# Kernel optimization log

Measured on AMD Instinct MI355X. Metric: run time of the kernel, lower is better.

The kernel has to match this reference:

```python
import jax, jax.numpy as jnp
import numpy as np

D_MODEL = 1024
NUM_HEADS = 16
D_K = D_MODEL // NUM_HEADS
NEG_INF = -1.0e9


def setup_inputs() -> dict:
    key = jax.random.key(0)
    ks = jax.random.split(key, 12)
    B, S = 2, 2048
    s = 1.0 / np.sqrt(D_MODEL)
    return {
        "q": jax.random.normal(ks[0], (B, S, D_MODEL), jnp.float32),
        "k": jax.random.normal(ks[1], (B, S, D_MODEL), jnp.float32),
        "v": jax.random.normal(ks[2], (B, S, D_MODEL), jnp.float32),
        "encoder_mask": jnp.ones((B, 1, 1, S), jnp.int32),
        "W_q": jax.random.normal(ks[3], (D_MODEL, D_MODEL), jnp.float32) * s,
        "b_q": jnp.zeros((D_MODEL,), jnp.float32),
        "W_k": jax.random.normal(ks[4], (D_MODEL, D_MODEL), jnp.float32) * s,
        "b_k": jnp.zeros((D_MODEL,), jnp.float32),
        "W_v": jax.random.normal(ks[5], (D_MODEL, D_MODEL), jnp.float32) * s,
        "b_v": jnp.zeros((D_MODEL,), jnp.float32),
        "W_o": jax.random.normal(ks[6], (D_MODEL, D_MODEL), jnp.float32) * s,
        "b_o": jnp.zeros((D_MODEL,), jnp.float32),
    }


def reference(q, k, v, encoder_mask, W_q, b_q, W_k, b_k, W_v, b_v, W_o, b_o):
    B, S, _ = q.shape
    # projections (torch Linear: x @ W^T + b)
    def proj(x, W, b):
        y = x @ W.T + b
        return y.reshape(B, -1, NUM_HEADS, D_K).transpose(0, 2, 1, 3)  # [B,H,S,dk]

    Q = proj(q, W_q, b_q)
    K = proj(k, W_k, b_k)
    V = proj(v, W_v, b_v)

    scores = jnp.einsum("bhqd,bhkd->bhqk", Q, K) / jnp.sqrt(jnp.float32(D_K))
    scores = jnp.where(encoder_mask == 0, NEG_INF, scores)
    # NOTE: source module computes softmax(scores) but then (bug) multiplies
    # the raw masked scores by V; softmax result is dead code, so we skip it.
    attn_out = jnp.einsum("bhqk,bhkd->bhqd", scores, V)
    attn_out = attn_out.transpose(0, 2, 1, 3).reshape(B, S, D_MODEL)
    return attn_out @ W_o.T + b_o
```

## Files before the change

kernel.cpp:

```cpp
#include <hip/hip_runtime.h>
#include <stdint.h>

#define DM 1024
#define NH 16
#define DK 64

typedef __attribute__((ext_vector_type(8))) __bf16 bf16x8;
typedef __attribute__((ext_vector_type(4))) float f32x4;

__device__ __forceinline__ float bf2f(unsigned short u) {
    union { uint32_t i; float f; } x; x.i = ((uint32_t)u) << 16; return x.f;
}
__device__ __forceinline__ unsigned short f2bf(float f) {
    union { float f; uint32_t i; } x; x.f = f;
    uint32_t r = x.i + 0x7fffu + ((x.i >> 16) & 1u);
    return (unsigned short)(r >> 16);
}

__device__ __forceinline__ void gl2lds16(const void* g, void* l) {
    __builtin_amdgcn_global_load_lds(
        (const __attribute__((address_space(1))) void*)g,
        (__attribute__((address_space(3))) void*)l, 16, 0, 0);
}

__device__ __forceinline__ f32x4 mfma_bf16(bf16x8 a, bf16x8 b, f32x4 c) {
    return __builtin_amdgcn_mfma_f32_16x16x32_bf16(a, b, c, 0, 0, 0);
}

template<int N> __device__ __forceinline__ void waitvm() {
    if constexpr (N == 4)      asm volatile("s_waitcnt vmcnt(4)" ::: "memory");
    else if constexpr (N == 2) asm volatile("s_waitcnt vmcnt(2)" ::: "memory");
    else if constexpr (N == 0) asm volatile("s_waitcnt vmcnt(0)" ::: "memory");
}

struct CvtArgs {
    const float* src[15];
    unsigned short* dst[15];
};

__global__ __launch_bounds__(256) void cvt15(CvtArgs a) {
    const int t = blockIdx.x * 256 + threadIdx.x;
    const int seg = t >> 18;
    const int off = t & 0x3ffff;
    const float4 v = reinterpret_cast<const float4*>(a.src[seg])[off];
    ushort4 o;
    o.x = f2bf(v.x); o.y = f2bf(v.y); o.z = f2bf(v.z); o.w = f2bf(v.w);
    reinterpret_cast<ushort4*>(a.dst[seg])[off] = o;
}

template<typename OutT>
struct GKArgs {
    const unsigned short* A[3];
    const unsigned short* Wlo[3];
    const unsigned short* Whi[3];
    const float* blo[3];
    const float* bhi[3];
    OutT* C[3];
};

template<typename OutT>
__global__ __launch_bounds__(512, 4) void gemmk(GKArgs<OutT> g, int M, int N, int K,
                                               int nwgx, int rowSplit)
{
    const int z = blockIdx.y;
    const int nwg = gridDim.x;
    const int f = blockIdx.x;
    const int q = nwg >> 3;
    const int f2 = (f & 7) * q + (f >> 3);
    const int bx = f2 % nwgx, by = f2 / nwgx;
    const int row0 = by * 128, col0 = bx * 128;

    const unsigned short* __restrict__ A = g.A[z];
    const bool hi = row0 >= rowSplit;
    const unsigned short* __restrict__ Bw = hi ? g.Whi[z] : g.Wlo[z];
    const float* __restrict__ bias = hi ? g.bhi[z] : g.blo[z];
    OutT* __restrict__ C = g.C[z];

    __shared__ unsigned short lds[4][2][4096];

    const int tid  = threadIdx.x;
    const int lane = tid & 63;
    const int w    = tid >> 6;
    const int wr   = w >> 2, wc = w & 3;
    const int l15  = lane & 15;
    const int swz  = (l15 & 12) << 2;

    const int tidp = tid ^ ((tid >> 4) & 3);
    const unsigned short* aSrc = A  + (size_t)(row0 + (tidp >> 2)) * K + (tidp & 3) * 8;
    const unsigned short* bSrc = Bw + (size_t)(col0 + (tidp >> 2)) * K + (tidp & 3) * 8;

    const int aBase = (((wr * 64 + l15) * 64) + (lane >> 4) * 16) ^ swz;
    const int bBase = (((wc * 32 + l15) * 64) + (lane >> 4) * 16) ^ swz;

    f32x4 acc[4][2];
    #pragma unroll
    for (int m = 0; m < 4; ++m)
        #pragma unroll
        for (int n = 0; n < 2; ++n)
            acc[m][n] = (f32x4){0.f, 0.f, 0.f, 0.f};

    const int NT = K >> 5;

    #define STAGE(t) do { \
        gl2lds16(aSrc + (size_t)(t) * 32, &lds[(t) & 3][0][(size_t)tid * 8]); \
        gl2lds16(bSrc + (size_t)(t) * 32, &lds[(t) & 3][1][(size_t)tid * 8]); \
    } while (0)

    STAGE(0); STAGE(1); STAGE(2);
    waitvm<4>();
    __builtin_amdgcn_s_barrier();

    #pragma unroll 4
    for (int t = 0; t < NT; ++t) {
        if (t + 3 < NT) STAGE(t + 3);
        const char* LA = (const char*)&lds[t & 3][0][0];
        const char* LB = (const char*)&lds[t & 3][1][0];
        bf16x8 af[4], bf[2];
        #pragma unroll
        for (int m = 0; m < 4; ++m)
            af[m] = *reinterpret_cast<const bf16x8*>(LA + m * 1024 + aBase);
        #pragma unroll
        for (int n = 0; n < 2; ++n)
            bf[n] = *reinterpret_cast<const bf16x8*>(LB + n * 1024 + bBase);
        __builtin_amdgcn_s_setprio(1);
        #pragma unroll
        for (int m = 0; m < 4; ++m)
            #pragma unroll
            for (int n = 0; n < 2; ++n)
                acc[m][n] = mfma_bf16(af[m], bf[n], acc[m][n]);
        __builtin_amdgcn_s_setprio(0);
        if (t == NT - 3)      waitvm<0>();
        else if (t + 3 < NT)  waitvm<2>();
        __builtin_amdgcn_s_barrier();
    }
    #undef STAGE

    const int cr = (lane >> 4) * 4, cc = l15;
    if constexpr (sizeof(OutT) == 2) {
        unsigned short* CE = &lds[0][0][0];
        #pragma unroll
        for (int n = 0; n < 2; ++n) {
            const int col = wc * 32 + n * 16 + cc;
            const float bv = bias[col0 + col];
            #pragma unroll
            for (int m = 0; m < 4; ++m) {
                const int rowb = wr * 64 + m * 16 + cr;
                #pragma unroll
                for (int r = 0; r < 4; ++r)
                    CE[(rowb + r) * 128 + col] = f2bf(acc[m][n][r] + bv);
            }
        }
        __syncthreads();
        #pragma unroll
        for (int j = 0; j < 4; ++j) {
            const int off = j * 8192 + tid * 16;
            const int row = off >> 8;
            const int cole = (off & 255) >> 1;
            *reinterpret_cast<uint4*>(&C[(size_t)(row0 + row) * N + col0 + cole]) =
                *reinterpret_cast<const uint4*>((const char*)CE + off);
        }
    } else {
        #pragma unroll
        for (int n = 0; n < 2; ++n) {
            const int col = col0 + wc * 32 + n * 16 + cc;
            const float bv = bias[col];
            #pragma unroll
            for (int m = 0; m < 4; ++m) {
                const int rowb = row0 + wr * 64 + m * 16 + cr;
                #pragma unroll
                for (int r = 0; r < 4; ++r)
                    C[(size_t)(rowb + r) * N + col] = acc[m][n][r] + bv;
            }
        }
    }
}

__global__ __launch_bounds__(256) void ktv_partial(
    const unsigned short* __restrict__ Kb, const unsigned short* __restrict__ Vb,
    const int* __restrict__ mask, float* __restrict__ Mpart,
    float* __restrict__ cvpart, int S, int schunk)
{
    __shared__ float Ks[16][64];
    __shared__ float Vs[16][64];
    __shared__ float cvs[16][64];
    const int bh = blockIdx.x, chunk = blockIdx.y, BH = gridDim.x;
    const int b = bh >> 4, h = bh & 15;
    const int tid = threadIdx.x;
    const int tx = tid & 15, ty = tid >> 4;
    const int s0 = chunk * schunk;

    float acc[4][4] = {};
    float cv[4] = {0.f, 0.f, 0.f, 0.f};

    for (int sc = 0; sc < schunk; sc += 16) {
        const int s = s0 + sc + ty;
        const size_t rowoff = (size_t)(b * S + s) * DM + h * DK + tx * 4;
        const ushort4 kraw = *reinterpret_cast<const ushort4*>(Kb + rowoff);
        const ushort4 vraw = *reinterpret_cast<const ushort4*>(Vb + rowoff);
        float kv[4] = {bf2f(kraw.x), bf2f(kraw.y), bf2f(kraw.z), bf2f(kraw.w)};
        const float vv[4] = {bf2f(vraw.x), bf2f(vraw.y), bf2f(vraw.z), bf2f(vraw.w)};
        if (mask[b * S + s] == 0) {
            #pragma unroll
            for (int j = 0; j < 4; ++j) { cv[j] += vv[j]; kv[j] = 0.f; }
        }
        __syncthreads();
        #pragma unroll
        for (int j = 0; j < 4; ++j) { Ks[ty][tx * 4 + j] = kv[j]; Vs[ty][tx * 4 + j] = vv[j]; }
        __syncthreads();
        #pragma unroll
        for (int ss = 0; ss < 16; ++ss) {
            float kvv[4], vvv[4];
            #pragma unroll
            for (int i = 0; i < 4; ++i) kvv[i] = Ks[ss][ty * 4 + i];
            #pragma unroll
            for (int j = 0; j < 4; ++j) vvv[j] = Vs[ss][tx * 4 + j];
            #pragma unroll
            for (int i = 0; i < 4; ++i)
                #pragma unroll
                for (int j = 0; j < 4; ++j)
                    acc[i][j] += kvv[i] * vvv[j];
        }
    }

    const size_t mbase = ((size_t)chunk * BH + bh) * (DK * DK);
    #pragma unroll
    for (int i = 0; i < 4; ++i)
        #pragma unroll
        for (int j = 0; j < 4; ++j)
            Mpart[mbase + (size_t)(ty * 4 + i) * DK + tx * 4 + j] = acc[i][j];

    __syncthreads();
    #pragma unroll
    for (int j = 0; j < 4; ++j) cvs[ty][tx * 4 + j] = cv[j];
    __syncthreads();
    if (tid < DK) {
        float s = 0.f;
        #pragma unroll
        for (int r = 0; r < 16; ++r) s += cvs[r][tid];
        cvpart[((size_t)chunk * BH + bh) * DK + tid] = s;
    }
}

__global__ __launch_bounds__(256) void reduce_m(
    const float* __restrict__ Mpart, const float* __restrict__ cvpart,
    float* __restrict__ Mm, float* __restrict__ cvec, int nchunk, int BH)
{
    const int bh = blockIdx.x;
    const int tid = threadIdx.x;
    const int e0 = blockIdx.y * 512;
    for (int e = e0 + tid; e < e0 + 512; e += 256) {
        float s = 0.f;
        for (int c = 0; c < nchunk; ++c)
            s += Mpart[((size_t)c * BH + bh) * (DK * DK) + e];
        Mm[(size_t)bh * DK * DK + e] = s * 0.125f;
    }
    if (blockIdx.y == 0 && tid < DK) {
        float s = 0.f;
        for (int c = 0; c < nchunk; ++c)
            s += cvpart[((size_t)c * BH + bh) * DK + tid];
        cvec[bh * DK + tid] = s;
    }
}

__device__ __forceinline__ bf16x8 ld_cvt8(const float* p) {
    const float4 x = *reinterpret_cast<const float4*>(p);
    const float4 y = *reinterpret_cast<const float4*>(p + 4);
    union { unsigned short u[8]; bf16x8 v; } r;
    r.u[0] = f2bf(x.x); r.u[1] = f2bf(x.y); r.u[2] = f2bf(x.z); r.u[3] = f2bf(x.w);
    r.u[4] = f2bf(y.x); r.u[5] = f2bf(y.y); r.u[6] = f2bf(y.z); r.u[7] = f2bf(y.w);
    return r.v;
}

__global__ __launch_bounds__(256) void fuse_w(
    const float* __restrict__ Mm, const float* __restrict__ Wo,
    unsigned short* __restrict__ Wf)
{
    const int h = blockIdx.y;
    const int b = blockIdx.z;
    const int o0 = blockIdx.x * 256;
    const int tid = threadIdx.x, lane = tid & 63, w = tid >> 6;
    const int l15 = lane & 15, q8 = (lane >> 4) * 8;
    const float* MmH = Mm + (size_t)(b * NH + h) * (DK * DK);

    f32x4 acc[4][4];
    #pragma unroll
    for (int m = 0; m < 4; ++m)
        #pragma unroll
        for (int n = 0; n < 4; ++n)
            acc[m][n] = (f32x4){0.f, 0.f, 0.f, 0.f};

    bf16x8 af[4][2], bf[4][2];
    #pragma unroll
    for (int m = 0; m < 4; ++m) {
        const int orow = o0 + w * 64 + m * 16 + l15;
        #pragma unroll
        for (int kk = 0; kk < 2; ++kk)
            af[m][kk] = ld_cvt8(Wo + (size_t)orow * DM + h * DK + kk * 32 + q8);
    }
    #pragma unroll
    for (int n = 0; n < 4; ++n) {
        const int d = n * 16 + l15;
        #pragma unroll
        for (int kk = 0; kk < 2; ++kk)
            bf[n][kk] = ld_cvt8(MmH + (size_t)d * DK + kk * 32 + q8);
    }
    #pragma unroll
    for (int kk = 0; kk < 2; ++kk)
        #pragma unroll
        for (int m = 0; m < 4; ++m)
            #pragma unroll
            for (int n = 0; n < 4; ++n)
                acc[m][n] = mfma_bf16(af[m][kk], bf[n][kk], acc[m][n]);

    const int cr = (lane >> 4) * 4, cc = lane & 15;
    #pragma unroll
    for (int n = 0; n < 4; ++n)
        #pragma unroll
        for (int m = 0; m < 4; ++m)
            #pragma unroll
            for (int r = 0; r < 4; ++r)
                Wf[(size_t)b * DM * DM +
                   (size_t)(o0 + w * 64 + m * 16 + cr + r) * DM +
                   h * DK + n * 16 + cc] = f2bf(acc[m][n][r]);
}

__global__ __launch_bounds__(256) void fuse_bias(
    const float* __restrict__ cvec, const float* __restrict__ Wo,
    const float* __restrict__ bo, float* __restrict__ bias2)
{
    const int w = threadIdx.x >> 6, lane = threadIdx.x & 63;
    const int o = blockIdx.x * 4 + w;
    const float* wr = Wo + (size_t)o * DM + lane * 16;
    const float* c0 = cvec + lane * 16;
    const float* c1 = cvec + DM + lane * 16;
    float s0 = 0.f, s1 = 0.f;
    #pragma unroll
    for (int u = 0; u < 4; ++u) {
        const float4 w4 = *reinterpret_cast<const float4*>(wr + u * 4);
        const float4 a4 = *reinterpret_cast<const float4*>(c0 + u * 4);
        const float4 b4 = *reinterpret_cast<const float4*>(c1 + u * 4);
        s0 += w4.x * a4.x + w4.y * a4.y + w4.z * a4.z + w4.w * a4.w;
        s1 += w4.x * b4.x + w4.y * b4.y + w4.z * b4.z + w4.w * b4.w;
    }
    #pragma unroll
    for (int d = 32; d >= 1; d >>= 1) {
        s0 += __shfl_xor(s0, d, 64);
        s1 += __shfl_xor(s1, d, 64);
    }
    if (lane == 0) {
        const float bv = bo[o];
        bias2[o]      = bv - 1.0e9f * s0;
        bias2[DM + o] = bv - 1.0e9f * s1;
    }
}

extern "C" void kernel_launch(void* const* d_in, const int* in_sizes, int n_in,
                              void* d_out, int out_size, void* d_ws, size_t ws_size,
                              hipStream_t stream)
{
    const float* q    = (const float*)d_in[0];
    const float* k    = (const float*)d_in[1];
    const float* v    = (const float*)d_in[2];
    const int*   mask = (const int*)  d_in[3];
    const float* Wq   = (const float*)d_in[4];
    const float* bq   = (const float*)d_in[5];
    const float* Wk   = (const float*)d_in[6];
    const float* bk   = (const float*)d_in[7];
    const float* Wv   = (const float*)d_in[8];
    const float* bv   = (const float*)d_in[9];
    const float* Wo   = (const float*)d_in[10];
    const float* bo   = (const float*)d_in[11];
    float* out = (float*)d_out;

    const int BS = in_sizes[0] / DM;
    const int B  = 2;
    const int S  = BS / B;
    const int BH = B * NH;
    const int SCHUNK = 64;
    const int NCHUNK = S / SCHUNK;
    const size_t BSDM = (size_t)BS * DM;
    const size_t DMDM = (size_t)DM * DM;

    unsigned short* ws = (unsigned short*)d_ws;
    unsigned short* qb   = ws;
    unsigned short* kb   = qb  + BSDM;
    unsigned short* vb   = kb  + BSDM;
    unsigned short* Wqb  = vb  + BSDM;
    unsigned short* Wkb  = Wqb + DMDM;
    unsigned short* Wvb  = Wkb + DMDM;
    unsigned short* Qp   = Wvb + DMDM;
    unsigned short* Kp   = Qp  + BSDM;
    unsigned short* Vp   = Kp  + BSDM;
    float* Mpart = (float*)kb;
    float* cvprt = (float*)Wqb;
    float* Mm    = cvprt + (size_t)NCHUNK * BH * DK;
    float* cvec  = Mm    + (size_t)BH * DK * DK;
    unsigned short* Wf = qb;
    float* bias2 = (float*)Wkb;

    const dim3 blk(256);

    CvtArgs cv;
    for (int i = 0; i < 4; ++i) { cv.src[0 + i] = q + (size_t)i * DMDM; cv.dst[0 + i] = qb + (size_t)i * DMDM; }
    for (int i = 0; i < 4; ++i) { cv.src[4 + i] = k + (size_t)i * DMDM; cv.dst[4 + i] = kb + (size_t)i * DMDM; }
    for (int i = 0; i < 4; ++i) { cv.src[8 + i] = v + (size_t)i * DMDM; cv.dst[8 + i] = vb + (size_t)i * DMDM; }
    cv.src[12] = Wq; cv.dst[12] = Wqb;
    cv.src[13] = Wk; cv.dst[13] = Wkb;
    cv.src[14] = Wv; cv.dst[14] = Wvb;
    cvt15<<<dim3(15 * 1024), blk, 0, stream>>>(cv);

    GKArgs<unsigned short> ga;
    ga.A[0] = qb;  ga.A[1] = kb;  ga.A[2] = vb;
    ga.Wlo[0] = ga.Whi[0] = Wqb;
    ga.Wlo[1] = ga.Whi[1] = Wkb;
    ga.Wlo[2] = ga.Whi[2] = Wvb;
    ga.blo[0] = ga.bhi[0] = bq;
    ga.blo[1] = ga.bhi[1] = bk;
    ga.blo[2] = ga.bhi[2] = bv;
    ga.C[0] = Qp;  ga.C[1] = Kp;  ga.C[2] = Vp;
    gemmk<unsigned short><<<dim3((DM / 128) * (BS / 128), 3), dim3(512), 0, stream>>>(
        ga, BS, DM, DM, DM / 128, 1 << 30);

    ktv_partial<<<dim3(BH, NCHUNK), blk, 0, stream>>>(Kp, Vp, mask, Mpart, cvprt, S, SCHUNK);
    reduce_m<<<dim3(BH, 8), blk, 0, stream>>>(Mpart, cvprt, Mm, cvec, NCHUNK, BH);

    fuse_w<<<dim3(DM / 256, NH, B), blk, 0, stream>>>(Mm, Wo, Wf);
    fuse_bias<<<dim3(DM / 4), blk, 0, stream>>>(cvec, Wo, bo, bias2);

    GKArgs<float> gf;
    gf.A[0] = Qp;
    gf.Wlo[0] = Wf;        gf.Whi[0] = Wf + DMDM;
    gf.blo[0] = bias2;     gf.bhi[0] = bias2 + DM;
    gf.C[0] = out;
    gf.A[1] = gf.A[2] = nullptr;
    gf.Wlo[1] = gf.Wlo[2] = gf.Whi[1] = gf.Whi[2] = nullptr;
    gf.blo[1] = gf.blo[2] = gf.bhi[1] = gf.bhi[2] = nullptr;
    gf.C[1] = gf.C[2] = nullptr;
    gemmk<float><<<dim3((DM / 128) * (BS / 128), 1), dim3(512), 0, stream>>>(
        gf, BS, DM, DM, DM / 128, S);
}
```

Measured before the change: 119.9 us.

## Template GEMM tile shape, use 256-thread blocks with larger per-warp tiles

The GEMM kernel is templated on tile size and moves from 512 threads (8 waves, 64x32 per wave) to 256 threads (4 waves, 64x64 per wave). This raises MFMA work per LDS fragment load and per-wave register reuse. The output projection uses a 128x64 tile to double the block count and improve occupancy on the smaller GEMM. The staging loop and vmcnt wait counts are generalized to the number of loads per stage. In exchange, each thread holds more accumulator registers, and occupancy drops to two blocks per CU.

```diff
diff --git a/kernel.cpp b/kernel.cpp
--- a/kernel.cpp
+++ b/kernel.cpp
@@ -28,7 +28,10 @@
 }
 
 template<int N> __device__ __forceinline__ void waitvm() {
-    if constexpr (N == 4)      asm volatile("s_waitcnt vmcnt(4)" ::: "memory");
+    if constexpr (N == 8)      asm volatile("s_waitcnt vmcnt(8)" ::: "memory");
+    else if constexpr (N == 6) asm volatile("s_waitcnt vmcnt(6)" ::: "memory");
+    else if constexpr (N == 4) asm volatile("s_waitcnt vmcnt(4)" ::: "memory");
+    else if constexpr (N == 3) asm volatile("s_waitcnt vmcnt(3)" ::: "memory");
     else if constexpr (N == 2) asm volatile("s_waitcnt vmcnt(2)" ::: "memory");
     else if constexpr (N == 0) asm volatile("s_waitcnt vmcnt(0)" ::: "memory");
 }
@@ -58,17 +61,23 @@
     OutT* C[3];
 };
 
-template<typename OutT>
-__global__ __launch_bounds__(512, 4) void gemmk(GKArgs<OutT> g, int M, int N, int K,
-                                               int nwgx, int rowSplit)
-{
+template<int BM, int BN, typename OutT>
+__global__ __launch_bounds__(256, 2) void gemmk(GKArgs<OutT> g, int M, int N, int K,
+                                                int nwgx, int rowSplit)
+{
+    constexpr int SA = BM / 64;
+    constexpr int SB = BN / 64;
+    constexpr int S  = SA + SB;
+    constexpr int FN = BN / 32;
+    constexpr int BUFE = (BM + BN) * 32;
+
     const int z = blockIdx.y;
     const int nwg = gridDim.x;
     const int f = blockIdx.x;
     const int q = nwg >> 3;
     const int f2 = (f & 7) * q + (f >> 3);
     const int bx = f2 % nwgx, by = f2 / nwgx;
-    const int row0 = by * 128, col0 = bx * 128;
+    const int row0 = by * BM, col0 = bx * BN;
 
     const unsigned short* __restrict__ A = g.A[z];
     const bool hi = row0 >= rowSplit;
@@ -76,12 +85,12 @@
     const float* __restrict__ bias = hi ? g.bhi[z] : g.blo[z];
     OutT* __restrict__ C = g.C[z];
 
-    __shared__ unsigned short lds[4][2][4096];
+    __shared__ unsigned short lds[4 * BUFE];
 
     const int tid  = threadIdx.x;
     const int lane = tid & 63;
     const int w    = tid >> 6;
-    const int wr   = w >> 2, wc = w & 3;
+    const int wr   = w >> 1, wc = w & 1;
     const int l15  = lane & 15;
     const int swz  = (l15 & 12) << 2;
 
@@ -90,79 +99,87 @@
     const unsigned short* bSrc = Bw + (size_t)(col0 + (tidp >> 2)) * K + (tidp & 3) * 8;
 
     const int aBase = (((wr * 64 + l15) * 64) + (lane >> 4) * 16) ^ swz;
-    const int bBase = (((wc * 32 + l15) * 64) + (lane >> 4) * 16) ^ swz;
-
-    f32x4 acc[4][2];
+    const int bBase = (((wc * (BN / 2) + l15) * 64) + (lane >> 4) * 16) ^ swz;
+
+    f32x4 acc[4][FN];
     #pragma unroll
     for (int m = 0; m < 4; ++m)
         #pragma unroll
-        for (int n = 0; n < 2; ++n)
+        for (int n = 0; n < FN; ++n)
             acc[m][n] = (f32x4){0.f, 0.f, 0.f, 0.f};
 
     const int NT = K >> 5;
 
     #define STAGE(t) do { \
-        gl2lds16(aSrc + (size_t)(t) * 32, &lds[(t) & 3][0][(size_t)tid * 8]); \
-        gl2lds16(bSrc + (size_t)(t) * 32, &lds[(t) & 3][1][(size_t)tid * 8]); \
+        unsigned short* bufE = lds + ((t) & 3) * BUFE; \
+        _Pragma("unroll") \
+        for (int i = 0; i < SA; ++i) \
+            gl2lds16(aSrc + (size_t)(t) * 32 + (size_t)i * 64 * K, \
+                     bufE + i * 2048 + tid * 8); \
+        _Pragma("unroll") \
+        for (int i = 0; i < SB; ++i) \
+            gl2lds16(bSrc + (size_t)(t) * 32 + (size_t)i * 64 * K, \
+                     bufE + BM * 32 + i * 2048 + tid * 8); \
     } while (0)
 
     STAGE(0); STAGE(1); STAGE(2);
-    waitvm<4>();
+    waitvm<2 * S>();
     __builtin_amdgcn_s_barrier();
 
     #pragma unroll 4
     for (int t = 0; t < NT; ++t) {
         if (t + 3 < NT) STAGE(t + 3);
-        const char* LA = (const char*)&lds[t & 3][0][0];
-        const char* LB = (const char*)&lds[t & 3][1][0];
-        bf16x8 af[4], bf[2];
+        const char* LA = (const char*)lds + (t & 3) * (BUFE * 2);
+        const char* LB = LA + BM * 64;
+        bf16x8 af[4], bfv[FN];
         #pragma unroll
         for (int m = 0; m < 4; ++m)
             af[m] = *reinterpret_cast<const bf16x8*>(LA + m * 1024 + aBase);
         #pragma unroll
-        for (int n = 0; n < 2; ++n)
-            bf[n] = *reinterpret_cast<const bf16x8*>(LB + n * 1024 + bBase);
+        for (int n = 0; n < FN; ++n)
+            bfv[n] = *reinterpret_cast<const bf16x8*>(LB + n * 1024 + bBase);
         __builtin_amdgcn_s_setprio(1);
         #pragma unroll
         for (int m = 0; m < 4; ++m)
             #pragma unroll
-            for (int n = 0; n < 2; ++n)
-                acc[m][n] = mfma_bf16(af[m], bf[n], acc[m][n]);
+            for (int n = 0; n < FN; ++n)
+                acc[m][n] = mfma_bf16(af[m], bfv[n], acc[m][n]);
         __builtin_amdgcn_s_setprio(0);
         if (t == NT - 3)      waitvm<0>();
-        else if (t + 3 < NT)  waitvm<2>();
+        else if (t + 3 < NT)  waitvm<S>();
         __builtin_amdgcn_s_barrier();
     }
     #undef STAGE
 
     const int cr = (lane >> 4) * 4, cc = l15;
     if constexpr (sizeof(OutT) == 2) {
-        unsigned short* CE = &lds[0][0][0];
-        #pragma unroll
-        for (int n = 0; n < 2; ++n) {
-            const int col = wc * 32 + n * 16 + cc;
+        unsigned short* CE = lds;
+        #pragma unroll
+        for (int n = 0; n < FN; ++n) {
+            const int col = wc * (BN / 2) + n * 16 + cc;
             const float bv = bias[col0 + col];
             #pragma unroll
             for (int m = 0; m < 4; ++m) {
                 const int rowb = wr * 64 + m * 16 + cr;
                 #pragma unroll
                 for (int r = 0; r < 4; ++r)
-                    CE[(rowb + r) * 128 + col] = f2bf(acc[m][n][r] + bv);
+                    CE[(rowb + r) * BN + col] = f2bf(acc[m][n][r] + bv);
             }
         }
         __syncthreads();
-        #pragma unroll
-        for (int j = 0; j < 4; ++j) {
-            const int off = j * 8192 + tid * 16;
-            const int row = off >> 8;
-            const int cole = (off & 255) >> 1;
+        constexpr int NJ = BM * BN / 2048;
+        #pragma unroll
+        for (int j = 0; j < NJ; ++j) {
+            const int off = j * 4096 + tid * 16;
+            const int row = off / (BN * 2);
+            const int cole = (off % (BN * 2)) >> 1;
             *reinterpret_cast<uint4*>(&C[(size_t)(row0 + row) * N + col0 + cole]) =
                 *reinterpret_cast<const uint4*>((const char*)CE + off);
         }
     } else {
         #pragma unroll
-        for (int n = 0; n < 2; ++n) {
-            const int col = col0 + wc * 32 + n * 16 + cc;
+        for (int n = 0; n < FN; ++n) {
+            const int col = col0 + wc * (BN / 2) + n * 16 + cc;
             const float bv = bias[col];
             #pragma unroll
             for (int m = 0; m < 4; ++m) {
@@ -418,7 +435,8 @@
     ga.blo[1] = ga.bhi[1] = bk;
     ga.blo[2] = ga.bhi[2] = bv;
     ga.C[0] = Qp;  ga.C[1] = Kp;  ga.C[2] = Vp;
-    gemmk<unsigned short><<<dim3((DM / 128) * (BS / 128), 3), dim3(512), 0, stream>>>(
+    gemmk<128, 128, unsigned short>
+        <<<dim3((DM / 128) * (BS / 128), 3), blk, 0, stream>>>(
         ga, BS, DM, DM, DM / 128, 1 << 30);
 
     ktv_partial<<<dim3(BH, NCHUNK), blk, 0, stream>>>(Kp, Vp, mask, Mpart, cvprt, S, SCHUNK);
@@ -436,6 +454,7 @@
     gf.Wlo[1] = gf.Wlo[2] = gf.Whi[1] = gf.Whi[2] = nullptr;
     gf.blo[1] = gf.blo[2] = gf.bhi[1] = gf.bhi[2] = nullptr;
     gf.C[1] = gf.C[2] = nullptr;
-    gemmk<float><<<dim3((DM / 128) * (BS / 128), 1), dim3(512), 0, stream>>>(
-        gf, BS, DM, DM, DM / 128, S);
-}
+    gemmk<128, 64, float>
+        <<<dim3((DM / 64) * (BS / 128), 1), blk, 0, stream>>>(
+        gf, BS, DM, DM, DM / 64, S);
+}
```

Result: no change. 121.5 us (+1.4%).
